# Performance work log

Measured on AMD Instinct MI355X. Metric: run time of the kernel, lower is better.

## Reference

```python
import jax, jax.numpy as jnp
import numpy as np

H = 4       # hidden size
IN = 906    # input size
B = 128
T = 512


def _lstm_dir(xp, W_hh):
    """Run a single-direction LSTM. xp: [B, T, 4H] precomputed input projection
    (x @ W_ih^T + b_ih + b_hh). Returns hidden states [B, T, H].
    Torch gate order: i, f, g, o."""
    Bb = xp.shape[0]
    h0 = jnp.zeros((Bb, H), xp.dtype)
    c0 = jnp.zeros((Bb, H), xp.dtype)

    def step(carry, g_t):
        h, c = carry
        g = g_t + h @ W_hh.T                      # [B, 4H]
        i, f, gg, o = jnp.split(g, 4, axis=-1)
        i = jax.nn.sigmoid(i)
        f = jax.nn.sigmoid(f)
        gg = jnp.tanh(gg)
        o = jax.nn.sigmoid(o)
        c = f * c + i * gg
        h = o * jnp.tanh(c)
        return (h, c), h

    xs = jnp.swapaxes(xp, 0, 1)                   # [T, B, 4H]
    _, hs = jax.lax.scan(step, (h0, c0), xs)      # hs: [T, B, H]
    return jnp.swapaxes(hs, 0, 1)                 # [B, T, H]


def setup_inputs() -> dict:
    key = jax.random.key(0)
    ks = jax.random.split(key, 12)
    s = 1.0 / np.sqrt(H)  # torch nn.LSTM init scale
    d = {
        "x": jax.random.normal(ks[0], (B, T, IN), jnp.float32),
        "W_ih_f": jax.random.normal(ks[1], (4 * H, IN), jnp.float32) * s,
        "W_hh_f": jax.random.normal(ks[2], (4 * H, H), jnp.float32) * s,
        "b_ih_f": jax.random.normal(ks[3], (4 * H,), jnp.float32) * s,
        "b_hh_f": jax.random.normal(ks[4], (4 * H,), jnp.float32) * s,
        "W_ih_b": jax.random.normal(ks[5], (4 * H, IN), jnp.float32) * s,
        "W_hh_b": jax.random.normal(ks[6], (4 * H, H), jnp.float32) * s,
        "b_ih_b": jax.random.normal(ks[7], (4 * H,), jnp.float32) * s,
        "b_hh_b": jax.random.normal(ks[8], (4 * H,), jnp.float32) * s,
        "W_out": jax.random.normal(ks[9], (2, 2 * H), jnp.float32) * s,
        "b_out": jax.random.normal(ks[10], (2,), jnp.float32) * s,
    }
    return d


def reference(x, W_ih_f, W_hh_f, b_ih_f, b_hh_f, W_ih_b, W_hh_b, b_ih_b, b_hh_b, W_out, b_out):
    # forward direction
    xp_f = x @ W_ih_f.T + (b_ih_f + b_hh_f)       # [B, T, 4H]
    out_f = _lstm_dir(xp_f, W_hh_f)               # [B, T, H]
    # backward direction: process reversed sequence, then flip back to align time
    xr = x[:, ::-1]
    xp_b = xr @ W_ih_b.T + (b_ih_b + b_hh_b)
    out_b = _lstm_dir(xp_b, W_hh_b)[:, ::-1]      # [B, T, H]
    # r_out[:, -1, :] = concat(fwd last step, bwd output at last time index)
    last = jnp.concatenate([out_f[:, -1], out_b[:, -1]], axis=-1)  # [B, 2H]
    return last @ W_out.T + b_out                 # [B, 2]
```

## Files before the change

kernel.cpp:

```cpp
#include <hip/hip_runtime.h>

#define IN 906
#define TT 512
#define NB 128

__device__ __forceinline__ float fsigm(float x) {
    float e = __builtin_amdgcn_exp2f(-1.4426950408889634f * x);
    return __builtin_amdgcn_rcpf(1.f + e);
}
__device__ __forceinline__ float ftanh(float x) {
    float e = __builtin_amdgcn_exp2f(-2.8853900817779268f * x);
    return 2.f * __builtin_amdgcn_rcpf(1.f + e) - 1.f;
}
template <int M>
__device__ __forceinline__ float quad_bcast(float v) {
    constexpr int ctrl = M | (M << 2) | (M << 4) | (M << 6);
    return __int_as_float(
        __builtin_amdgcn_mov_dpp(__float_as_int(v), ctrl, 0xf, 0xf, true));
}

__global__ __launch_bounds__(256)
void gemm_xp(const float* __restrict__ x, const float* __restrict__ W,
             const float* __restrict__ b1, const float* __restrict__ b2,
             float* __restrict__ xp)
{
    __shared__ float sx[2][32][132];
    __shared__ float sw[2][32][16];
    const int tid = threadIdx.x;
    const size_t rowbase = (size_t)blockIdx.x * 128;

    const int srow = tid >> 1;
    const int sseg = tid & 1;
    const float* __restrict__ xrow = x + (rowbase + srow) * IN + sseg * 16;
    const int wout = tid >> 4;
    const int wcc  = (tid & 15) * 2;

    const int kh  = tid >> 7;
    const int rem = tid & 127;
    const int rg  = rem >> 2;
    const int og  = rem & 3;
    const int r0  = rg * 4;

    float2 xr[8];
    float2 wr;
    float acc[4][4];
#pragma unroll
    for (int r = 0; r < 4; ++r)
#pragma unroll
        for (int m = 0; m < 4; ++m) acc[r][m] = 0.f;

    auto load_chunk = [&](int c) {
        const int k0 = c * 32;
        if (c < 28) {
#pragma unroll
            for (int q = 0; q < 8; ++q)
                xr[q] = *(const float2*)(xrow + k0 + q * 2);
            wr = *(const float2*)(W + wout * IN + k0 + wcc);
        } else {
#pragma unroll
            for (int q = 0; q < 8; ++q) {
                int col = k0 + sseg * 16 + q * 2;
                xr[q].x = (col     < IN) ? xrow[k0 + q * 2]     : 0.f;
                xr[q].y = (col + 1 < IN) ? xrow[k0 + q * 2 + 1] : 0.f;
            }
            int colw = k0 + wcc;
            wr.x = (colw     < IN) ? W[wout * IN + colw]     : 0.f;
            wr.y = (colw + 1 < IN) ? W[wout * IN + colw + 1] : 0.f;
        }
    };
    auto write_chunk = [&](int buf) {
#pragma unroll
        for (int q = 0; q < 8; ++q) {
            int cc = sseg * 16 + q * 2;
            sx[buf][cc][srow]     = xr[q].x;
            sx[buf][cc + 1][srow] = xr[q].y;
        }
        sw[buf][wcc][wout]     = wr.x;
        sw[buf][wcc + 1][wout] = wr.y;
    };
    auto compute = [&](int buf) {
#pragma unroll
        for (int cc2 = 0; cc2 < 16; ++cc2) {
            const int cc = kh * 16 + cc2;
            float4 xv = *(const float4*)&sx[buf][cc][r0];
            float4 wv = *(const float4*)&sw[buf][cc][og * 4];
            acc[0][0] = fmaf(xv.x, wv.x, acc[0][0]);
            acc[0][1] = fmaf(xv.x, wv.y, acc[0][1]);
            acc[0][2] = fmaf(xv.x, wv.z, acc[0][2]);
            acc[0][3] = fmaf(xv.x, wv.w, acc[0][3]);
            acc[1][0] = fmaf(xv.y, wv.x, acc[1][0]);
            acc[1][1] = fmaf(xv.y, wv.y, acc[1][1]);
            acc[1][2] = fmaf(xv.y, wv.z, acc[1][2]);
            acc[1][3] = fmaf(xv.y, wv.w, acc[1][3]);
            acc[2][0] = fmaf(xv.z, wv.x, acc[2][0]);
            acc[2][1] = fmaf(xv.z, wv.y, acc[2][1]);
            acc[2][2] = fmaf(xv.z, wv.z, acc[2][2]);
            acc[2][3] = fmaf(xv.z, wv.w, acc[2][3]);
            acc[3][0] = fmaf(xv.w, wv.x, acc[3][0]);
            acc[3][1] = fmaf(xv.w, wv.y, acc[3][1]);
            acc[3][2] = fmaf(xv.w, wv.z, acc[3][2]);
            acc[3][3] = fmaf(xv.w, wv.w, acc[3][3]);
        }
    };

    load_chunk(0);
    write_chunk(0);
    __syncthreads();
    for (int c = 0; c < 29; ++c) {
        if (c < 28) load_chunk(c + 1);
        compute(c & 1);
        if (c < 28) write_chunk((c + 1) & 1);
        __syncthreads();
    }

    float* red = &sx[0][0][0];
    if (kh == 1) {
#pragma unroll
        for (int r = 0; r < 4; ++r)
#pragma unroll
            for (int m = 0; m < 4; ++m)
                red[(r * 4 + m) * 128 + rem] = acc[r][m];
    }
    __syncthreads();
    if (kh == 0) {
#pragma unroll
        for (int r = 0; r < 4; ++r) {
            const size_t row = rowbase + r0 + r;
#pragma unroll
            for (int m = 0; m < 4; ++m) {
                const int j = og * 4 + m;
                float v = acc[r][m] + red[(r * 4 + m) * 128 + rem];
                xp[row * 16 + m * 4 + og] = v + b1[j] + b2[j];
            }
        }
    }
}

__global__ __launch_bounds__(256)
void frec(const float* __restrict__ xp, const float* __restrict__ x,
          const float* __restrict__ Whh, const float* __restrict__ Wb,
          const float* __restrict__ bb1, const float* __restrict__ bb2,
          const float* __restrict__ Wout, const float* __restrict__ bout,
          float* __restrict__ out)
{
    __shared__ float bg[16][12];
    const int tid = threadIdx.x;

    float h0 = 0.f, h1 = 0.f, h2 = 0.f, h3 = 0.f;

    if (tid >= 64) {
        const int gl = tid - 64;
        const int r  = gl >> 4;
        const int bq = gl & 15;
        const int b  = blockIdx.x * 16 + bq;
        const int gr = (r < 4) ? r : r + 4;
        const float2* __restrict__ xr  = (const float2*)(x + ((size_t)b * TT + (TT - 1)) * IN);
        const float2* __restrict__ wrp = (const float2*)(Wb + gr * IN);
        float s0 = 0.f, s1 = 0.f;
        int j = 0;
        for (; j + 8 <= 453; j += 8) {
#pragma unroll
            for (int u = 0; u < 8; ++u) {
                float2 a = xr[j + u];
                float2 w = wrp[j + u];
                s0 = fmaf(a.x, w.x, s0);
                s1 = fmaf(a.y, w.y, s1);
            }
        }
        for (; j < 453; ++j) {
            float2 a = xr[j];
            float2 w = wrp[j];
            s0 = fmaf(a.x, w.x, s0);
            s1 = fmaf(a.y, w.y, s1);
        }
        bg[bq][r] = s0 + s1 + bb1[gr] + bb2[gr];
    } else {
        const int k = tid & 3;
        const int b = blockIdx.x * 16 + (tid >> 2);

        float Wi[4], Wf4[4], Wg[4], Wo[4];
#pragma unroll
        for (int m = 0; m < 4; ++m) {
            Wi[m]  = Whh[(k)      * 4 + m];
            Wf4[m] = Whh[(4 + k)  * 4 + m];
            Wg[m]  = Whh[(8 + k)  * 4 + m];
            Wo[m]  = Whh[(12 + k) * 4 + m];
        }

        const float4* __restrict__ xq = (const float4*)xp;
        const size_t base = (size_t)b * TT * 4 + k;

        float4 pf[16];
#pragma unroll
        for (int i = 0; i < 16; ++i) pf[i] = xq[base + (size_t)i * 4];

        float c = 0.f;
        for (int t = 0; t < TT; t += 16) {
#pragma unroll
            for (int u = 0; u < 16; ++u) {
                float4 cur = pf[u];
                int tn = t + 16 + u;
                int tc = (tn < TT) ? tn : (TT - 1);
                pf[u] = xq[base + (size_t)tc * 4];

                float gi = cur.x + h0 * Wi[0]  + h1 * Wi[1]  + h2 * Wi[2]  + h3 * Wi[3];
                float gf = cur.y + h0 * Wf4[0] + h1 * Wf4[1] + h2 * Wf4[2] + h3 * Wf4[3];
                float gg = cur.z + h0 * Wg[0]  + h1 * Wg[1]  + h2 * Wg[2]  + h3 * Wg[3];
                float go = cur.w + h0 * Wo[0]  + h1 * Wo[1]  + h2 * Wo[2]  + h3 * Wo[3];

                float si = fsigm(gi);
                float sf = fsigm(gf);
                float tg = ftanh(gg);
                float so = fsigm(go);

                c = sf * c + si * tg;
                float h = so * ftanh(c);

                h0 = quad_bcast<0>(h);
                h1 = quad_bcast<1>(h);
                h2 = quad_bcast<2>(h);
                h3 = quad_bcast<3>(h);
            }
        }
    }

    __syncthreads();

    if (tid < 64) {
        const int k  = tid & 3;
        const int bq = tid >> 2;
        const int b  = blockIdx.x * 16 + bq;

        float gib = bg[bq][k];
        float ggb = bg[bq][4 + k];
        float gob = bg[bq][8 + k];
        float hbk = fsigm(gob) * ftanh(fsigm(gib) * ftanh(ggb));
        float hb0 = quad_bcast<0>(hbk);
        float hb1 = quad_bcast<1>(hbk);
        float hb2 = quad_bcast<2>(hbk);
        float hb3 = quad_bcast<3>(hbk);

        float o0 = bout[0]
                 + h0  * Wout[0]  + h1  * Wout[1]  + h2  * Wout[2]  + h3  * Wout[3]
                 + hb0 * Wout[4]  + hb1 * Wout[5]  + hb2 * Wout[6]  + hb3 * Wout[7];
        float o1 = bout[1]
                 + h0  * Wout[8]  + h1  * Wout[9]  + h2  * Wout[10] + h3  * Wout[11]
                 + hb0 * Wout[12] + hb1 * Wout[13] + hb2 * Wout[14] + hb3 * Wout[15];

        if (k == 0) {
            out[b * 2 + 0] = o0;
            out[b * 2 + 1] = o1;
        }
    }
}

extern "C" void kernel_launch(void* const* d_in, const int* in_sizes, int n_in,
                              void* d_out, int out_size, void* d_ws, size_t ws_size,
                              hipStream_t stream)
{
    const float* x    = (const float*)d_in[0];
    const float* Wihf = (const float*)d_in[1];
    const float* Whhf = (const float*)d_in[2];
    const float* bihf = (const float*)d_in[3];
    const float* bhhf = (const float*)d_in[4];
    const float* Wihb = (const float*)d_in[5];
    const float* bihb = (const float*)d_in[7];
    const float* bhhb = (const float*)d_in[8];
    const float* Wout = (const float*)d_in[9];
    const float* bout = (const float*)d_in[10];

    float* xp = (float*)d_ws;

    gemm_xp<<<512, 256, 0, stream>>>(x, Wihf, bihf, bhhf, xp);
    frec<<<8, 256, 0, stream>>>(xp, x, Whhf, Wihb, bihb, bhhb, Wout, bout,
                                (float*)d_out);
}
```

Measured before the change: 433.1 us.

## Halve GEMM row tile to 64 and add triple-buffered shared-memory pipeline

```diff
diff --git a/kernel.cpp b/kernel.cpp
--- a/kernel.cpp
+++ b/kernel.cpp
@@ -24,14 +24,15 @@
              const float* __restrict__ b1, const float* __restrict__ b2,
              float* __restrict__ xp)
 {
-    __shared__ float sx[2][32][132];
-    __shared__ float sw[2][32][16];
+    __shared__ float sx[3][32][68];
+    __shared__ float sw[3][32][16];
+    __shared__ float red[8][128];
     const int tid = threadIdx.x;
-    const size_t rowbase = (size_t)blockIdx.x * 128;
-
-    const int srow = tid >> 1;
-    const int sseg = tid & 1;
-    const float* __restrict__ xrow = x + (rowbase + srow) * IN + sseg * 16;
+    const size_t rowbase = (size_t)blockIdx.x * 64;
+
+    const int srow = tid >> 2;
+    const int sseg = tid & 3;
+    const float* __restrict__ xrow = x + (rowbase + srow) * IN + sseg * 8;
     const int wout = tid >> 4;
     const int wcc  = (tid & 15) * 2;
 
@@ -39,13 +40,13 @@
     const int rem = tid & 127;
     const int rg  = rem >> 2;
     const int og  = rem & 3;
-    const int r0  = rg * 4;
-
-    float2 xr[8];
+    const int r0  = rg * 2;
+
+    float2 xr[4];
     float2 wr;
-    float acc[4][4];
-#pragma unroll
-    for (int r = 0; r < 4; ++r)
+    float acc[2][4];
+#pragma unroll
+    for (int r = 0; r < 2; ++r)
 #pragma unroll
         for (int m = 0; m < 4; ++m) acc[r][m] = 0.f;
 
@@ -53,25 +54,27 @@
         const int k0 = c * 32;
         if (c < 28) {
 #pragma unroll
-            for (int q = 0; q < 8; ++q)
+            for (int q = 0; q < 4; ++q)
                 xr[q] = *(const float2*)(xrow + k0 + q * 2);
             wr = *(const float2*)(W + wout * IN + k0 + wcc);
         } else {
 #pragma unroll
-            for (int q = 0; q < 8; ++q) {
-                int col = k0 + sseg * 16 + q * 2;
-                xr[q].x = (col     < IN) ? xrow[k0 + q * 2]     : 0.f;
-                xr[q].y = (col + 1 < IN) ? xrow[k0 + q * 2 + 1] : 0.f;
+            for (int q = 0; q < 4; ++q) {
+                int col = k0 + sseg * 8 + q * 2;
+                bool ok = (col < IN);
+                xr[q].x = ok ? xrow[k0 + q * 2]     : 0.f;
+                xr[q].y = ok ? xrow[k0 + q * 2 + 1] : 0.f;
             }
             int colw = k0 + wcc;
-            wr.x = (colw     < IN) ? W[wout * IN + colw]     : 0.f;
-            wr.y = (colw + 1 < IN) ? W[wout * IN + colw + 1] : 0.f;
+            bool okw = (colw < IN);
+            wr.x = okw ? W[wout * IN + colw]     : 0.f;
+            wr.y = okw ? W[wout * IN + colw + 1] : 0.f;
         }
     };
     auto write_chunk = [&](int buf) {
 #pragma unroll
-        for (int q = 0; q < 8; ++q) {
-            int cc = sseg * 16 + q * 2;
+        for (int q = 0; q < 4; ++q) {
+            int cc = sseg * 8 + q * 2;
             sx[buf][cc][srow]     = xr[q].x;
             sx[buf][cc + 1][srow] = xr[q].y;
         }
@@ -82,7 +85,7 @@
 #pragma unroll
         for (int cc2 = 0; cc2 < 16; ++cc2) {
             const int cc = kh * 16 + cc2;
-            float4 xv = *(const float4*)&sx[buf][cc][r0];
+            float2 xv = *(const float2*)&sx[buf][cc][r0];
             float4 wv = *(const float4*)&sw[buf][cc][og * 4];
             acc[0][0] = fmaf(xv.x, wv.x, acc[0][0]);
             acc[0][1] = fmaf(xv.x, wv.y, acc[0][1]);
@@ -92,44 +95,36 @@
             acc[1][1] = fmaf(xv.y, wv.y, acc[1][1]);
             acc[1][2] = fmaf(xv.y, wv.z, acc[1][2]);
             acc[1][3] = fmaf(xv.y, wv.w, acc[1][3]);
-            acc[2][0] = fmaf(xv.z, wv.x, acc[2][0]);
-            acc[2][1] = fmaf(xv.z, wv.y, acc[2][1]);
-            acc[2][2] = fmaf(xv.z, wv.z, acc[2][2]);
-            acc[2][3] = fmaf(xv.z, wv.w, acc[2][3]);
-            acc[3][0] = fmaf(xv.w, wv.x, acc[3][0]);
-            acc[3][1] = fmaf(xv.w, wv.y, acc[3][1]);
-            acc[3][2] = fmaf(xv.w, wv.z, acc[3][2]);
-            acc[3][3] = fmaf(xv.w, wv.w, acc[3][3]);
         }
     };
 
-    load_chunk(0);
-    write_chunk(0);
+    load_chunk(0);  write_chunk(0);
+    load_chunk(1);  write_chunk(1);
     __syncthreads();
+
     for (int c = 0; c < 29; ++c) {
-        if (c < 28) load_chunk(c + 1);
-        compute(c & 1);
-        if (c < 28) write_chunk((c + 1) & 1);
+        if (c + 2 < 29) load_chunk(c + 2);
+        compute(c % 3);
+        if (c + 2 < 29) write_chunk((c + 2) % 3);
         __syncthreads();
     }
 
-    float* red = &sx[0][0][0];
     if (kh == 1) {
 #pragma unroll
-        for (int r = 0; r < 4; ++r)
+        for (int r = 0; r < 2; ++r)
 #pragma unroll
             for (int m = 0; m < 4; ++m)
-                red[(r * 4 + m) * 128 + rem] = acc[r][m];
+                red[r * 4 + m][rem] = acc[r][m];
     }
     __syncthreads();
     if (kh == 0) {
 #pragma unroll
-        for (int r = 0; r < 4; ++r) {
+        for (int r = 0; r < 2; ++r) {
             const size_t row = rowbase + r0 + r;
 #pragma unroll
             for (int m = 0; m < 4; ++m) {
                 const int j = og * 4 + m;
-                float v = acc[r][m] + red[(r * 4 + m) * 128 + rem];
+                float v = acc[r][m] + red[r * 4 + m][rem];
                 xp[row * 16 + m * 4 + og] = v + b1[j] + b2[j];
             }
         }
@@ -271,7 +266,7 @@
 
     float* xp = (float*)d_ws;
 
-    gemm_xp<<<512, 256, 0, stream>>>(x, Wihf, bihf, bhhf, xp);
+    gemm_xp<<<1024, 256, 0, stream>>>(x, Wihf, bihf, bhhf, xp);
     frec<<<8, 256, 0, stream>>>(xp, x, Whhf, Wihb, bihb, bhhb, Wout, bout,
                                 (float*)d_out);
 }
```

Result: slower. 450.5 us (+4.0%).

## Fuse projection GEMM and recurrence into one kernel with per-chunk readiness flags

Applied to the files above, without the earlier changes.

```diff
diff --git a/kernel.cpp b/kernel.cpp
--- a/kernel.cpp
+++ b/kernel.cpp
@@ -19,132 +19,144 @@
         __builtin_amdgcn_mov_dpp(__float_as_int(v), ctrl, 0xf, 0xf, true));
 }
 
+__device__ unsigned xp_flags[512];
+
+__global__ void zero_flags_k()
+{
+    xp_flags[threadIdx.x] = 0u;
+}
+
 __global__ __launch_bounds__(256)
-void gemm_xp(const float* __restrict__ x, const float* __restrict__ W,
-             const float* __restrict__ b1, const float* __restrict__ b2,
-             float* __restrict__ xp)
+void fused(const float* __restrict__ x,  const float* __restrict__ W,
+           const float* __restrict__ b1, const float* __restrict__ b2,
+           const float* __restrict__ Whh, const float* __restrict__ Wb,
+           const float* __restrict__ bb1, const float* __restrict__ bb2,
+           const float* __restrict__ Wout, const float* __restrict__ bout,
+           float* __restrict__ xp, float* __restrict__ out)
 {
     __shared__ float sx[2][32][132];
     __shared__ float sw[2][32][16];
-    const int tid = threadIdx.x;
-    const size_t rowbase = (size_t)blockIdx.x * 128;
-
-    const int srow = tid >> 1;
-    const int sseg = tid & 1;
-    const float* __restrict__ xrow = x + (rowbase + srow) * IN + sseg * 16;
-    const int wout = tid >> 4;
-    const int wcc  = (tid & 15) * 2;
-
-    const int kh  = tid >> 7;
-    const int rem = tid & 127;
-    const int rg  = rem >> 2;
-    const int og  = rem & 3;
-    const int r0  = rg * 4;
-
-    float2 xr[8];
-    float2 wr;
-    float acc[4][4];
-#pragma unroll
-    for (int r = 0; r < 4; ++r)
-#pragma unroll
-        for (int m = 0; m < 4; ++m) acc[r][m] = 0.f;
-
-    auto load_chunk = [&](int c) {
-        const int k0 = c * 32;
-        if (c < 28) {
-#pragma unroll
-            for (int q = 0; q < 8; ++q)
-                xr[q] = *(const float2*)(xrow + k0 + q * 2);
-            wr = *(const float2*)(W + wout * IN + k0 + wcc);
-        } else {
-#pragma unroll
-            for (int q = 0; q < 8; ++q) {
-                int col = k0 + sseg * 16 + q * 2;
-                xr[q].x = (col     < IN) ? xrow[k0 + q * 2]     : 0.f;
-                xr[q].y = (col + 1 < IN) ? xrow[k0 + q * 2 + 1] : 0.f;
-            }
-            int colw = k0 + wcc;
-            wr.x = (colw     < IN) ? W[wout * IN + colw]     : 0.f;
-            wr.y = (colw + 1 < IN) ? W[wout * IN + colw + 1] : 0.f;
-        }
-    };
-    auto write_chunk = [&](int buf) {
-#pragma unroll
-        for (int q = 0; q < 8; ++q) {
-            int cc = sseg * 16 + q * 2;
-            sx[buf][cc][srow]     = xr[q].x;
-            sx[buf][cc + 1][srow] = xr[q].y;
-        }
-        sw[buf][wcc][wout]     = wr.x;
-        sw[buf][wcc + 1][wout] = wr.y;
-    };
-    auto compute = [&](int buf) {
-#pragma unroll
-        for (int cc2 = 0; cc2 < 16; ++cc2) {
-            const int cc = kh * 16 + cc2;
-            float4 xv = *(const float4*)&sx[buf][cc][r0];
-            float4 wv = *(const float4*)&sw[buf][cc][og * 4];
-            acc[0][0] = fmaf(xv.x, wv.x, acc[0][0]);
-            acc[0][1] = fmaf(xv.x, wv.y, acc[0][1]);
-            acc[0][2] = fmaf(xv.x, wv.z, acc[0][2]);
-            acc[0][3] = fmaf(xv.x, wv.w, acc[0][3]);
-            acc[1][0] = fmaf(xv.y, wv.x, acc[1][0]);
-            acc[1][1] = fmaf(xv.y, wv.y, acc[1][1]);
-            acc[1][2] = fmaf(xv.y, wv.z, acc[1][2]);
-            acc[1][3] = fmaf(xv.y, wv.w, acc[1][3]);
-            acc[2][0] = fmaf(xv.z, wv.x, acc[2][0]);
-            acc[2][1] = fmaf(xv.z, wv.y, acc[2][1]);
-            acc[2][2] = fmaf(xv.z, wv.z, acc[2][2]);
-            acc[2][3] = fmaf(xv.z, wv.w, acc[2][3]);
-            acc[3][0] = fmaf(xv.w, wv.x, acc[3][0]);
-            acc[3][1] = fmaf(xv.w, wv.y, acc[3][1]);
-            acc[3][2] = fmaf(xv.w, wv.z, acc[3][2]);
-            acc[3][3] = fmaf(xv.w, wv.w, acc[3][3]);
-        }
-    };
-
-    load_chunk(0);
-    write_chunk(0);
-    __syncthreads();
-    for (int c = 0; c < 29; ++c) {
-        if (c < 28) load_chunk(c + 1);
-        compute(c & 1);
-        if (c < 28) write_chunk((c + 1) & 1);
-        __syncthreads();
-    }
-
-    float* red = &sx[0][0][0];
-    if (kh == 1) {
-#pragma unroll
-        for (int r = 0; r < 4; ++r)
-#pragma unroll
-            for (int m = 0; m < 4; ++m)
-                red[(r * 4 + m) * 128 + rem] = acc[r][m];
-    }
-    __syncthreads();
-    if (kh == 0) {
-#pragma unroll
-        for (int r = 0; r < 4; ++r) {
-            const size_t row = rowbase + r0 + r;
-#pragma unroll
-            for (int m = 0; m < 4; ++m) {
-                const int j = og * 4 + m;
-                float v = acc[r][m] + red[(r * 4 + m) * 128 + rem];
-                xp[row * 16 + m * 4 + og] = v + b1[j] + b2[j];
-            }
-        }
-    }
-}
-
-__global__ __launch_bounds__(256)
-void frec(const float* __restrict__ xp, const float* __restrict__ x,
-          const float* __restrict__ Whh, const float* __restrict__ Wb,
-          const float* __restrict__ bb1, const float* __restrict__ bb2,
-          const float* __restrict__ Wout, const float* __restrict__ bout,
-          float* __restrict__ out)
-{
     __shared__ float bg[16][12];
     const int tid = threadIdx.x;
+
+    if (blockIdx.x >= 8) {
+        const int p   = (int)blockIdx.x - 8;
+        const int tcp = p >> 7;
+        const int bp  = p & 127;
+        const size_t rowbase = (size_t)bp * 512 + (size_t)tcp * 128;
+
+        const int srow = tid >> 1;
+        const int sseg = tid & 1;
+        const float* __restrict__ xrow = x + (rowbase + srow) * IN + sseg * 16;
+        const int wout = tid >> 4;
+        const int wcc  = (tid & 15) * 2;
+
+        const int kh  = tid >> 7;
+        const int rem = tid & 127;
+        const int rg  = rem >> 2;
+        const int og  = rem & 3;
+        const int r0  = rg * 4;
+
+        float2 xr[8];
+        float2 wr;
+        float acc[4][4];
+#pragma unroll
+        for (int r = 0; r < 4; ++r)
+#pragma unroll
+            for (int m = 0; m < 4; ++m) acc[r][m] = 0.f;
+
+        auto load_chunk = [&](int c) {
+            const int k0 = c * 32;
+            if (c < 28) {
+#pragma unroll
+                for (int q = 0; q < 8; ++q)
+                    xr[q] = *(const float2*)(xrow + k0 + q * 2);
+                wr = *(const float2*)(W + wout * IN + k0 + wcc);
+            } else {
+#pragma unroll
+                for (int q = 0; q < 8; ++q) {
+                    int col = k0 + sseg * 16 + q * 2;
+                    xr[q].x = (col     < IN) ? xrow[k0 + q * 2]     : 0.f;
+                    xr[q].y = (col + 1 < IN) ? xrow[k0 + q * 2 + 1] : 0.f;
+                }
+                int colw = k0 + wcc;
+                wr.x = (colw     < IN) ? W[wout * IN + colw]     : 0.f;
+                wr.y = (colw + 1 < IN) ? W[wout * IN + colw + 1] : 0.f;
+            }
+        };
+        auto write_chunk = [&](int buf) {
+#pragma unroll
+            for (int q = 0; q < 8; ++q) {
+                int cc = sseg * 16 + q * 2;
+                sx[buf][cc][srow]     = xr[q].x;
+                sx[buf][cc + 1][srow] = xr[q].y;
+            }
+            sw[buf][wcc][wout]     = wr.x;
+            sw[buf][wcc + 1][wout] = wr.y;
+        };
+        auto compute = [&](int buf) {
+#pragma unroll
+            for (int cc2 = 0; cc2 < 16; ++cc2) {
+                const int cc = kh * 16 + cc2;
+                float4 xv = *(const float4*)&sx[buf][cc][r0];
+                float4 wv = *(const float4*)&sw[buf][cc][og * 4];
+                acc[0][0] = fmaf(xv.x, wv.x, acc[0][0]);
+                acc[0][1] = fmaf(xv.x, wv.y, acc[0][1]);
+                acc[0][2] = fmaf(xv.x, wv.z, acc[0][2]);
+                acc[0][3] = fmaf(xv.x, wv.w, acc[0][3]);
+                acc[1][0] = fmaf(xv.y, wv.x, acc[1][0]);
+                acc[1][1] = fmaf(xv.y, wv.y, acc[1][1]);
+                acc[1][2] = fmaf(xv.y, wv.z, acc[1][2]);
+                acc[1][3] = fmaf(xv.y, wv.w, acc[1][3]);
+                acc[2][0] = fmaf(xv.z, wv.x, acc[2][0]);
+                acc[2][1] = fmaf(xv.z, wv.y, acc[2][1]);
+                acc[2][2] = fmaf(xv.z, wv.z, acc[2][2]);
+                acc[2][3] = fmaf(xv.z, wv.w, acc[2][3]);
+                acc[3][0] = fmaf(xv.w, wv.x, acc[3][0]);
+                acc[3][1] = fmaf(xv.w, wv.y, acc[3][1]);
+                acc[3][2] = fmaf(xv.w, wv.z, acc[3][2]);
+                acc[3][3] = fmaf(xv.w, wv.w, acc[3][3]);
+            }
+        };
+
+        load_chunk(0);
+        write_chunk(0);
+        __syncthreads();
+        for (int c = 0; c < 29; ++c) {
+            if (c < 28) load_chunk(c + 1);
+            compute(c & 1);
+            if (c < 28) write_chunk((c + 1) & 1);
+            __syncthreads();
+        }
+
+        float* red = &sx[0][0][0];
+        if (kh == 1) {
+#pragma unroll
+            for (int r = 0; r < 4; ++r)
+#pragma unroll
+                for (int m = 0; m < 4; ++m)
+                    red[(r * 4 + m) * 128 + rem] = acc[r][m];
+        }
+        __syncthreads();
+        if (kh == 0) {
+#pragma unroll
+            for (int r = 0; r < 4; ++r) {
+                const size_t row = rowbase + r0 + r;
+#pragma unroll
+                for (int m = 0; m < 4; ++m) {
+                    const int j = og * 4 + m;
+                    float v = acc[r][m] + red[(r * 4 + m) * 128 + rem];
+                    xp[row * 16 + m * 4 + og] = v + b1[j] + b2[j];
+                }
+            }
+        }
+
+        __syncthreads();
+        if (tid == 0)
+            __hip_atomic_store(&xp_flags[p], 1u, __ATOMIC_RELEASE,
+                               __HIP_MEMORY_SCOPE_AGENT);
+        return;
+    }
 
     float h0 = 0.f, h1 = 0.f, h2 = 0.f, h3 = 0.f;
 
@@ -178,6 +190,16 @@
         const int k = tid & 3;
         const int b = blockIdx.x * 16 + (tid >> 2);
 
+        auto wait_flag = [&](int tcw) {
+            const int fi = tcw * 128 + b;
+            for (;;) {
+                unsigned f = __hip_atomic_load(&xp_flags[fi], __ATOMIC_ACQUIRE,
+                                               __HIP_MEMORY_SCOPE_AGENT);
+                if (__all(f != 0u)) break;
+                __builtin_amdgcn_s_sleep(8);
+            }
+        };
+
         float Wi[4], Wf4[4], Wg[4], Wo[4];
 #pragma unroll
         for (int m = 0; m < 4; ++m) {
@@ -190,12 +212,17 @@
         const float4* __restrict__ xq = (const float4*)xp;
         const size_t base = (size_t)b * TT * 4 + k;
 
+        wait_flag(0);
+        wait_flag(1);
+
         float4 pf[16];
 #pragma unroll
         for (int i = 0; i < 16; ++i) pf[i] = xq[base + (size_t)i * 4];
 
         float c = 0.f;
         for (int t = 0; t < TT; t += 16) {
+            if (t == 240) wait_flag(2);
+            if (t == 368) wait_flag(3);
 #pragma unroll
             for (int u = 0; u < 16; ++u) {
                 float4 cur = pf[u];
@@ -271,7 +298,8 @@
 
     float* xp = (float*)d_ws;
 
-    gemm_xp<<<512, 256, 0, stream>>>(x, Wihf, bihf, bhhf, xp);
-    frec<<<8, 256, 0, stream>>>(xp, x, Whhf, Wihb, bihb, bhhb, Wout, bout,
-                                (float*)d_out);
-}
+    zero_flags_k<<<1, 512, 0, stream>>>();
+    fused<<<520, 256, 0, stream>>>(x, Wihf, bihf, bhhf,
+                                   Whhf, Wihb, bihb, bhhb, Wout, bout,
+                                   xp, (float*)d_out);
+}
```

After: 458.6 us. 5.9% more time.
